# Kernel optimization log

Hardware: AMD Instinct MI355X
Metric: run time of the kernel (lower is better)

## Reference

```python
import jax, jax.numpy as jnp
import numpy as np

HIDDEN = 4096
NUM_HEADS = 32
NUM_KV_HEADS = 8
HEAD_DIM = 128
EPS = 1e-6
ROPE_THETA = 1000000.0
T = 2048


def setup_inputs() -> dict:
    key = jax.random.key(0)
    k1, k2, k3, k4, k5 = jax.random.split(key, 5)
    q_size = NUM_HEADS * HEAD_DIM
    kv_size = NUM_KV_HEADS * HEAD_DIM
    return {
        "positions": jnp.arange(T, dtype=jnp.int32),
        "hidden_states": jax.random.normal(k1, (T, HIDDEN), dtype=jnp.float32),
        "w_qkv": jax.random.normal(k2, (HIDDEN, q_size + 2 * kv_size), dtype=jnp.float32) * 0.02,
        "w_o": jax.random.normal(k3, (q_size, HIDDEN), dtype=jnp.float32) * 0.02,
        "q_norm_w": jnp.ones((HEAD_DIM,), dtype=jnp.float32) + 0.01 * jax.random.normal(k4, (HEAD_DIM,), dtype=jnp.float32),
        "k_norm_w": jnp.ones((HEAD_DIM,), dtype=jnp.float32) + 0.01 * jax.random.normal(k5, (HEAD_DIM,), dtype=jnp.float32),
    }


def _rms_norm(x, w, eps=EPS):
    # x: [..., head_dim], normalize over last dim
    var = jnp.mean(jnp.square(x), axis=-1, keepdims=True)
    return x * jax.lax.rsqrt(var + eps) * w


def _apply_rope(x, positions):
    # neox-style rotate-half RoPE, rotary_dim == head_dim
    d = x.shape[-1]
    inv_freq = 1.0 / (ROPE_THETA ** (jnp.arange(0, d, 2, dtype=jnp.float32) / d))
    freqs = positions.astype(jnp.float32)[:, None] * inv_freq[None, :]  # [T, d/2]
    cos = jnp.cos(freqs)[:, None, :]  # [T, 1, d/2]
    sin = jnp.sin(freqs)[:, None, :]
    x1, x2 = jnp.split(x, 2, axis=-1)
    return jnp.concatenate([x1 * cos - x2 * sin, x2 * cos + x1 * sin], axis=-1)


def reference(positions, hidden_states, w_qkv, w_o, q_norm_w, k_norm_w):
    num_tokens = hidden_states.shape[0]
    q_size = NUM_HEADS * HEAD_DIM
    kv_size = NUM_KV_HEADS * HEAD_DIM
    group = NUM_HEADS // NUM_KV_HEADS

    qkv = hidden_states @ w_qkv  # [T, q+2kv]
    q = qkv[:, :q_size].reshape(num_tokens, NUM_HEADS, HEAD_DIM)
    k = qkv[:, q_size:q_size + kv_size].reshape(num_tokens, NUM_KV_HEADS, HEAD_DIM)
    v = qkv[:, q_size + kv_size:].reshape(num_tokens, NUM_KV_HEADS, HEAD_DIM)

    q = _rms_norm(q, q_norm_w)
    k = _rms_norm(k, k_norm_w)
    q = _apply_rope(q, positions)
    k = _apply_rope(k, positions)

    scale = HEAD_DIM ** -0.5
    # GQA: group query heads over shared kv heads
    qg = q.reshape(num_tokens, NUM_KV_HEADS, group, HEAD_DIM)
    scores = jnp.einsum("tkgd,skd->kgts", qg * scale, k)  # [KH, G, T, S]
    causal = positions[:, None] >= positions[None, :]  # [T, S]
    scores = jnp.where(causal[None, None, :, :], scores, jnp.finfo(scores.dtype).min)
    probs = jax.nn.softmax(scores, axis=-1)
    out = jnp.einsum("kgts,skd->tkgd", probs, v)  # [T, KH, G, D]
    out = out.reshape(num_tokens, q_size)
    return out @ w_o
```

## Files before the change

kernel.cpp:

```cpp
#include <hip/hip_runtime.h>
#include <cstdint>
#include <cstddef>

#define T_TOK 2048
#define HID   4096
#define NQH   32
#define NKVH  8
#define HD    128
#define QKV_N 6144

typedef __bf16 bf16x8 __attribute__((ext_vector_type(8)));
typedef __bf16 bf16x4 __attribute__((ext_vector_type(4)));
typedef float  f32x4  __attribute__((ext_vector_type(4)));
typedef float  f32x16 __attribute__((ext_vector_type(16)));

#define AS1 __attribute__((address_space(1)))
#define AS3 __attribute__((address_space(3)))

__device__ __forceinline__ void gll16(const void* g, void* l) {
  __builtin_amdgcn_global_load_lds((const AS1 void*)g, (AS3 void*)l, 16, 0, 0);
}

__global__ __launch_bounds__(256) void k_convert(const float* __restrict__ in,
                                                 __bf16* __restrict__ out, int n4) {
  int i = blockIdx.x * 256 + threadIdx.x;
  if (i >= n4) return;
  float4 v = ((const float4*)in)[i];
  bf16x4 o;
  o[0] = (__bf16)v.x; o[1] = (__bf16)v.y; o[2] = (__bf16)v.z; o[3] = (__bf16)v.w;
  ((bf16x4*)out)[i] = o;
}

__global__ __launch_bounds__(256) void k_transpose(const float* __restrict__ in,
                                                   __bf16* __restrict__ out,
                                                   int R, int C) {
  __shared__ float tile[32][33];
  int c0 = blockIdx.x * 32, r0 = blockIdx.y * 32;
  int tx = threadIdx.x, ty = threadIdx.y;
#pragma unroll
  for (int k = 0; k < 4; ++k)
    tile[ty + k*8][tx] = in[(size_t)(r0 + ty + k*8) * C + c0 + tx];
  __syncthreads();
#pragma unroll
  for (int k = 0; k < 4; ++k)
    out[(size_t)(c0 + ty + k*8) * R + r0 + tx] = (__bf16)tile[tx][ty + k*8];
}

template <int NFR>
__global__ __launch_bounds__(512, 2) void k_gemm8(const __bf16* __restrict__ A,
                                                  const __bf16* __restrict__ Bt,
                                                  float* __restrict__ C,
                                                  int N, int K) {
  constexpr int BN   = 64 * NFR;
  constexpr int WN   = 16 * NFR;
  constexpr int NB   = NFR / 2;
  constexpr int NH   = NFR / 2;
  constexpr int BREG = BN * 64;
  constexpr int BUFSZ = 16384 + 2 * BREG;
  __shared__ alignas(16) char ldsb[2 * BUFSZ];
  const int tid = threadIdx.x;
  const int lane = tid & 63, w = tid >> 6;
  const int l16 = lane & 15, lg = lane >> 4;
  const int wm = w >> 2, wn = w & 3;

  const int x = blockIdx.x & 7, idx = blockIdx.x >> 3;
  const int bm = (x & 1) * 8 + (idx & 7);
  const int bn = (x >> 1) * 4 + (idx >> 3);

  const int rA = tid >> 2, pA = tid & 3;
  const __bf16* asrc = A + (size_t)(bm * 128 + rA) * K + ((pA ^ ((rA >> 1) & 3)) * 8);
  const __bf16* bsrc = Bt + (size_t)(bn * BN + rA) * K + ((pA ^ ((rA >> 1) & 3)) * 8);

#define RA_(buf, mk) (ldsb + (buf) * BUFSZ + (mk) * 8192)
#define RB_(buf, mk) (ldsb + (buf) * BUFSZ + 16384 + (mk) * BREG)
#define STG_A(buf, mk, kk) { gll16(asrc + (kk) + (mk) * 32, RA_(buf, mk) + w * 1024); }
#define STG_B(buf, mk, kk) { _Pragma("unroll") \
    for (int j = 0; j < NB; ++j) \
      gll16(bsrc + (size_t)j * 128 * K + (kk) + (mk) * 32, RB_(buf, mk) + j * 8192 + w * 1024); }
#define FRAG(base, row) (*(const bf16x8*)((base) + (row) * 64 + ((lg ^ (((row) >> 1) & 3)) << 4)))
#define WAITN() { if constexpr (NFR == 6) asm volatile("s_waitcnt vmcnt(4)" ::: "memory"); \
                  else                    asm volatile("s_waitcnt vmcnt(3)" ::: "memory"); }

  f32x4 acc[4][NFR] = {};
  const int nkt = K >> 6;

  STG_A(0, 0, 0); STG_B(0, 0, 0); STG_A(0, 1, 0); STG_B(0, 1, 0);

  for (int t = 0; t < nkt - 1; ++t) {
    const int cur = t & 1, nxt = cur ^ 1;
    const int kn = (t + 1) * 64;
    bf16x8 af[4], bf_[NH];

    STG_A(nxt, 0, kn);
    WAITN();
    __builtin_amdgcn_s_barrier();
    __builtin_amdgcn_sched_barrier(0);
#pragma unroll
    for (int i = 0; i < 4; ++i) af[i] = FRAG(RA_(cur, 0), wm * 64 + i * 16 + l16);
#pragma unroll
    for (int n = 0; n < NH; ++n) bf_[n] = FRAG(RB_(cur, 0), wn * WN + n * 16 + l16);
    __builtin_amdgcn_s_setprio(1);
#pragma unroll
    for (int i = 0; i < 4; ++i)
#pragma unroll
      for (int n = 0; n < NH; ++n)
        acc[i][n] = __builtin_amdgcn_mfma_f32_16x16x32_bf16(af[i], bf_[n], acc[i][n], 0, 0, 0);
    __builtin_amdgcn_s_setprio(0);
    __builtin_amdgcn_s_barrier();

#pragma unroll
    for (int n = 0; n < NH; ++n) bf_[n] = FRAG(RB_(cur, 0), wn * WN + (NH + n) * 16 + l16);
    STG_B(nxt, 0, kn);
    __builtin_amdgcn_s_barrier();
    __builtin_amdgcn_s_setprio(1);
#pragma unroll
    for (int i = 0; i < 4; ++i)
#pragma unroll
      for (int n = 0; n < NH; ++n)
        acc[i][NH + n] = __builtin_amdgcn_mfma_f32_16x16x32_bf16(af[i], bf_[n], acc[i][NH + n], 0, 0, 0);
    __builtin_amdgcn_s_setprio(0);
    __builtin_amdgcn_s_barrier();

    STG_A(nxt, 1, kn);
    WAITN();
    __builtin_amdgcn_s_barrier();
    __builtin_amdgcn_sched_barrier(0);
#pragma unroll
    for (int i = 0; i < 4; ++i) af[i] = FRAG(RA_(cur, 1), wm * 64 + i * 16 + l16);
#pragma unroll
    for (int n = 0; n < NH; ++n) bf_[n] = FRAG(RB_(cur, 1), wn * WN + n * 16 + l16);
    __builtin_amdgcn_s_setprio(1);
#pragma unroll
    for (int i = 0; i < 4; ++i)
#pragma unroll
      for (int n = 0; n < NH; ++n)
        acc[i][n] = __builtin_amdgcn_mfma_f32_16x16x32_bf16(af[i], bf_[n], acc[i][n], 0, 0, 0);
    __builtin_amdgcn_s_setprio(0);
    __builtin_amdgcn_s_barrier();

#pragma unroll
    for (int n = 0; n < NH; ++n) bf_[n] = FRAG(RB_(cur, 1), wn * WN + (NH + n) * 16 + l16);
    STG_B(nxt, 1, kn);
    __builtin_amdgcn_s_barrier();
    __builtin_amdgcn_s_setprio(1);
#pragma unroll
    for (int i = 0; i < 4; ++i)
#pragma unroll
      for (int n = 0; n < NH; ++n)
        acc[i][NH + n] = __builtin_amdgcn_mfma_f32_16x16x32_bf16(af[i], bf_[n], acc[i][NH + n], 0, 0, 0);
    __builtin_amdgcn_s_setprio(0);
    __builtin_amdgcn_s_barrier();
  }

  asm volatile("s_waitcnt vmcnt(0)" ::: "memory");
  __builtin_amdgcn_s_barrier();
  __builtin_amdgcn_sched_barrier(0);
  {
    const int cur = (nkt - 1) & 1;
#pragma unroll
    for (int mk = 0; mk < 2; ++mk) {
      bf16x8 aa[4], bb[NFR];
#pragma unroll
      for (int i = 0; i < 4; ++i) aa[i] = FRAG(RA_(cur, mk), wm * 64 + i * 16 + l16);
#pragma unroll
      for (int n = 0; n < NFR; ++n) bb[n] = FRAG(RB_(cur, mk), wn * WN + n * 16 + l16);
#pragma unroll
      for (int i = 0; i < 4; ++i)
#pragma unroll
        for (int n = 0; n < NFR; ++n)
          acc[i][n] = __builtin_amdgcn_mfma_f32_16x16x32_bf16(aa[i], bb[n], acc[i][n], 0, 0, 0);
    }
  }
#undef RA_
#undef RB_
#undef STG_A
#undef STG_B
#undef FRAG
#undef WAITN

#pragma unroll
  for (int mi = 0; mi < 4; ++mi)
#pragma unroll
    for (int ni = 0; ni < NFR; ++ni) {
      int row = bm * 128 + wm * 64 + mi * 16 + lg * 4;
      int col = bn * BN + wn * WN + ni * 16 + l16;
#pragma unroll
      for (int r = 0; r < 4; ++r)
        C[(size_t)(row + r) * N + col] = acc[mi][ni][r];
    }
}

__global__ __launch_bounds__(64) void k_norm_rope(const float* __restrict__ qkv,
                                                  const int* __restrict__ pos,
                                                  const float* __restrict__ qw,
                                                  const float* __restrict__ kw,
                                                  __bf16* __restrict__ qo,
                                                  __bf16* __restrict__ ko,
                                                  __bf16* __restrict__ vto) {
  const int slot = blockIdx.x;
  const int t    = blockIdx.y;
  const int i    = threadIdx.x;
  const int off  = (slot < 32) ? slot * 128
                 : (slot < 40) ? 4096 + (slot - 32) * 128
                                : 5120 + (slot - 40) * 128;
  const float* base = qkv + (size_t)t * QKV_N + off;
  float x1 = base[i], x2 = base[i + 64];
  if (slot >= 40) {
    __bf16* o = vto + ((size_t)(slot - 40) * HD) * T_TOK + t;
    o[(size_t)i * T_TOK] = (__bf16)x1;
    o[(size_t)(i + 64) * T_TOK] = (__bf16)x2;
    return;
  }
  float ss = x1 * x1 + x2 * x2;
#pragma unroll
  for (int m = 32; m >= 1; m >>= 1) ss += __shfl_xor(ss, m);
  float rinv = rsqrtf(ss * (1.0f / 128.0f) + 1e-6f);
  const float* wn = (slot < 32) ? qw : kw;
  float n1 = x1 * rinv * wn[i];
  float n2 = x2 * rinv * wn[i + 64];
  float fr = (float)pos[t] * expf((float)i * -0.21586735246819178f);
  float cs = cosf(fr), sn = sinf(fr);
  float o1 = n1 * cs - n2 * sn;
  float o2 = n2 * cs + n1 * sn;
  if (slot < 32) {
    const float QSC = 0.08838834764831845f * 1.4426950408889634f;
    __bf16* o = qo + ((size_t)t * NQH + slot) * HD;
    o[i] = (__bf16)(o1 * QSC);
    o[i + 64] = (__bf16)(o2 * QSC);
  } else {
    __bf16* o = ko + ((size_t)t * NKVH + (slot - 32)) * HD;
    o[i] = (__bf16)o1;
    o[i + 64] = (__bf16)o2;
  }
}

__global__ __launch_bounds__(256, 2) void k_attn(const __bf16* __restrict__ Q,
                                                 const __bf16* __restrict__ K,
                                                 const __bf16* __restrict__ Vt,
                                                 __bf16* __restrict__ O) {
  __shared__ alignas(16) __bf16 Ks[64 * 128];
  __shared__ alignas(16) __bf16 Vts[128 * 64];
  const int bid = blockIdx.x;
  const int kvh = bid & 7;
  const int qc  = bid >> 3;
  const int tid = threadIdx.x, lane = tid & 63, w = tid >> 6;
  const int l31 = lane & 31, hi = lane >> 5;
  const int h  = kvh * 4 + w;
  const int q0 = qc * 32;
  const int qrow = q0 + l31;
  char* Ksb = (char*)Ks;
  char* Vtb = (char*)Vts;

  bf16x8 qf[8];
  {
    const __bf16* qp = Q + ((size_t)qrow * NQH + h) * HD + hi * 8;
#pragma unroll
    for (int dc = 0; dc < 8; ++dc)
      qf[dc] = *(const bf16x8*)(qp + dc * 16);
  }

  size_t ksrc[4], vsrc[4];
#pragma unroll
  for (int j = 0; j < 4; ++j) {
    int kr = w * 16 + j * 4 + (lane >> 4);
    ksrc[j] = ((size_t)kr * NKVH + kvh) * HD + (size_t)(((lane & 15) ^ (kr & 15)) * 8);
    int vr = w * 32 + j * 8 + (lane >> 3);
    vsrc[j] = ((size_t)(kvh * HD + vr)) * T_TOK + (size_t)(((lane & 7) ^ (vr & 7)) * 8);
  }

  float m_run = -3.0e38f, l_run = 0.f;
  f32x16 ot[4] = {};

  const int ntiles = (qc >> 1) + 1;
  for (int tt = 0; tt < ntiles; ++tt) {
    const int s0 = tt * 64;
#pragma unroll
    for (int j = 0; j < 4; ++j) {
      gll16(K + (size_t)s0 * (NKVH * HD) + ksrc[j], Ksb + (w * 4 + j) * 1024);
      gll16(Vt + (size_t)s0 + vsrc[j], Vtb + (w * 4 + j) * 1024);
    }
    __syncthreads();

    f32x16 sac[2] = {};
#pragma unroll
    for (int hf = 0; hf < 2; ++hf) {
      int krow = hf * 32 + l31;
#pragma unroll
      for (int dc = 0; dc < 8; ++dc) {
        bf16x8 kf = *(const bf16x8*)(Ksb + krow * 256 + (((dc * 2 + hi) ^ (krow & 15)) * 16));
        sac[hf] = __builtin_amdgcn_mfma_f32_32x32x16_bf16(kf, qf[dc], sac[hf], 0, 0, 0);
      }
    }

    float pv[32];
    if (s0 + 64 > q0) {
#pragma unroll
      for (int hf = 0; hf < 2; ++hf)
#pragma unroll
        for (int r = 0; r < 16; ++r) {
          int kvg = s0 + hf * 32 + (r & 3) + ((r >> 2) * 8) + hi * 4;
          pv[hf * 16 + r] = (kvg > qrow) ? -3.0e38f : sac[hf][r];
        }
    } else {
#pragma unroll
      for (int hf = 0; hf < 2; ++hf)
#pragma unroll
        for (int r = 0; r < 16; ++r) pv[hf * 16 + r] = sac[hf][r];
    }
    float t16[16];
#pragma unroll
    for (int i = 0; i < 16; ++i) t16[i] = fmaxf(pv[i], pv[i + 16]);
#pragma unroll
    for (int i = 0; i < 8; ++i) t16[i] = fmaxf(t16[i], t16[i + 8]);
#pragma unroll
    for (int i = 0; i < 4; ++i) t16[i] = fmaxf(t16[i], t16[i + 4]);
    float mt = fmaxf(fmaxf(t16[0], t16[1]), fmaxf(t16[2], t16[3]));
    mt = fmaxf(mt, __shfl_xor(mt, 32));
    if (!__all(mt - m_run <= 10.0f)) {
      float m_new = fmaxf(m_run, mt);
      float corr = exp2f(m_run - m_new);
      l_run *= corr;
#pragma unroll
      for (int dt = 0; dt < 4; ++dt)
#pragma unroll
        for (int r = 0; r < 16; ++r) ot[dt][r] *= corr;
      m_run = m_new;
    }
#pragma unroll
    for (int i = 0; i < 32; ++i) pv[i] = exp2f(pv[i] - m_run);
#pragma unroll
    for (int i = 0; i < 16; ++i) t16[i] = pv[i] + pv[i + 16];
#pragma unroll
    for (int i = 0; i < 8; ++i) t16[i] += t16[i + 8];
#pragma unroll
    for (int i = 0; i < 4; ++i) t16[i] += t16[i + 4];
    float rs = (t16[0] + t16[1]) + (t16[2] + t16[3]);
    rs += __shfl_xor(rs, 32);
    l_run += rs;

    uint32_t wds[16];
#pragma unroll
    for (int i = 0; i < 16; ++i) {
      uint32_t r;
      asm("v_cvt_pk_bf16_f32 %0, %1, %2" : "=v"(r) : "v"(pv[2 * i]), "v"(pv[2 * i + 1]));
      wds[i] = r;
    }
#pragma unroll
    for (int c = 0; c < 4; ++c) {
      const int base = (c >> 1) * 8 + (c & 1) * 4;
      uint32_t sa = hi ? wds[base + 0] : wds[base + 2];
      uint32_t sb = hi ? wds[base + 1] : wds[base + 3];
      uint32_t ra = __shfl_xor(sa, 32);
      uint32_t rb = __shfl_xor(sb, 32);
      union { uint32_t u[4]; bf16x8 v; } pf;
      pf.u[0] = hi ? ra : wds[base + 0];
      pf.u[1] = hi ? rb : wds[base + 1];
      pf.u[2] = hi ? wds[base + 2] : ra;
      pf.u[3] = hi ? wds[base + 3] : rb;
#pragma unroll
      for (int dt = 0; dt < 4; ++dt) {
        int vrow = dt * 32 + l31;
        bf16x8 vf = *(const bf16x8*)(Vtb + vrow * 128 + (((c * 2 + hi) ^ (vrow & 7)) * 16));
        ot[dt] = __builtin_amdgcn_mfma_f32_32x32x16_bf16(vf, pf.v, ot[dt], 0, 0, 0);
      }
    }
    __syncthreads();
  }

  float inv = 1.0f / l_run;
  char* Ob = Ksb + w * 8192;
#pragma unroll
  for (int dt = 0; dt < 4; ++dt)
#pragma unroll
    for (int r = 0; r < 16; ++r) {
      int d = dt * 32 + (r & 3) + ((r >> 2) * 8) + hi * 4;
      *(__bf16*)(Ob + l31 * 256 + ((d * 2) ^ ((l31 & 7) << 4))) = (__bf16)(ot[dt][r] * inv);
    }
#pragma unroll
  for (int pass = 0; pass < 8; ++pass) {
    int q = pass * 4 + (lane >> 4);
    int ch = lane & 15;
    bf16x8 vvv = *(const bf16x8*)(Ob + q * 256 + ((ch ^ (q & 7)) * 16));
    *(bf16x8*)(O + ((size_t)(q0 + q) * NQH + h) * HD + ch * 8) = vvv;
  }
}

extern "C" void kernel_launch(void* const* d_in, const int* in_sizes, int n_in,
                              void* d_out, int out_size, void* d_ws, size_t ws_size,
                              hipStream_t stream) {
  const int*   positions = (const int*)d_in[0];
  const float* hidden    = (const float*)d_in[1];
  const float* w_qkv     = (const float*)d_in[2];
  const float* w_o       = (const float*)d_in[3];
  const float* q_norm    = (const float*)d_in[4];
  const float* k_norm    = (const float*)d_in[5];
  float* out = (float*)d_out;

  char* ws = (char*)d_ws;
  __bf16* wqkv_t   = (__bf16*)ws;
  __bf16* wo_t     = (__bf16*)(ws + 50331648);
  __bf16* hidden_b = (__bf16*)(ws + 83886080);
  float*  qkv      = (float*)(ws + 100663296);
  __bf16* qb  = (__bf16*)ws;
  __bf16* kb  = (__bf16*)(ws + 16777216);
  __bf16* vtb = (__bf16*)(ws + 20971520);
  __bf16* attn_o = hidden_b;

  k_convert<<<dim3((T_TOK * HID / 4 + 255) / 256), 256, 0, stream>>>(hidden, hidden_b, T_TOK * HID / 4);
  k_transpose<<<dim3(QKV_N / 32, HID / 32), dim3(32, 8), 0, stream>>>(w_qkv, wqkv_t, HID, QKV_N);
  k_transpose<<<dim3(HID / 32, HID / 32), dim3(32, 8), 0, stream>>>(w_o, wo_t, HID, HID);
  k_gemm8<6><<<dim3(256), 512, 0, stream>>>(hidden_b, wqkv_t, qkv, QKV_N, HID);
  k_norm_rope<<<dim3(48, T_TOK), 64, 0, stream>>>(qkv, positions, q_norm, k_norm, qb, kb, vtb);
  k_attn<<<dim3(512), 256, 0, stream>>>(qb, kb, vtb, attn_o);
  k_gemm8<4><<<dim3(256), 512, 0, stream>>>(attn_o, wo_t, out, HID, HID);
}
```

Measured before the change: 327.9 us.

## Vectorize weight transposes, split V transpose out, batch norm-rope per token

```diff
diff --git a/kernel.cpp b/kernel.cpp
--- a/kernel.cpp
+++ b/kernel.cpp
@@ -34,16 +34,48 @@
 __global__ __launch_bounds__(256) void k_transpose(const float* __restrict__ in,
                                                    __bf16* __restrict__ out,
                                                    int R, int C) {
-  __shared__ float tile[32][33];
-  int c0 = blockIdx.x * 32, r0 = blockIdx.y * 32;
-  int tx = threadIdx.x, ty = threadIdx.y;
-#pragma unroll
-  for (int k = 0; k < 4; ++k)
-    tile[ty + k*8][tx] = in[(size_t)(r0 + ty + k*8) * C + c0 + tx];
+  __shared__ float tile[64][33];
+  const int tid = threadIdx.x;
+  const int c0 = blockIdx.x * 32, r0 = blockIdx.y * 64;
+  const int ty = tid >> 3, tx = tid & 7;
+#pragma unroll
+  for (int k = 0; k < 2; ++k) {
+    float4 v = *(const float4*)&in[(size_t)(r0 + ty + k * 32) * C + c0 + tx * 4];
+    tile[ty + k * 32][tx * 4 + 0] = v.x;
+    tile[ty + k * 32][tx * 4 + 1] = v.y;
+    tile[ty + k * 32][tx * 4 + 2] = v.z;
+    tile[ty + k * 32][tx * 4 + 3] = v.w;
+  }
   __syncthreads();
-#pragma unroll
-  for (int k = 0; k < 4; ++k)
-    out[(size_t)(c0 + ty + k*8) * R + r0 + tx] = (__bf16)tile[tx][ty + k*8];
+  const int c = tid >> 3, rq = tid & 7;
+  bf16x8 o;
+#pragma unroll
+  for (int i = 0; i < 8; ++i) o[i] = (__bf16)tile[rq * 8 + i][c];
+  *(bf16x8*)&out[(size_t)(c0 + c) * R + r0 + rq * 8] = o;
+}
+
+__global__ __launch_bounds__(256) void k_vtrans(const float* __restrict__ qkv,
+                                                __bf16* __restrict__ vt) {
+  __shared__ float tile[64][33];
+  const int tid = threadIdx.x;
+  const int kvh = blockIdx.z;
+  const int d0 = blockIdx.x * 32;
+  const int t0 = blockIdx.y * 64;
+  const int ty = tid >> 3, tx = tid & 7;
+#pragma unroll
+  for (int k = 0; k < 2; ++k) {
+    float4 v = *(const float4*)&qkv[(size_t)(t0 + ty + k * 32) * QKV_N + 5120 + kvh * 128 + d0 + tx * 4];
+    tile[ty + k * 32][tx * 4 + 0] = v.x;
+    tile[ty + k * 32][tx * 4 + 1] = v.y;
+    tile[ty + k * 32][tx * 4 + 2] = v.z;
+    tile[ty + k * 32][tx * 4 + 3] = v.w;
+  }
+  __syncthreads();
+  const int d = tid >> 3, tq = tid & 7;
+  bf16x8 o;
+#pragma unroll
+  for (int i = 0; i < 8; ++i) o[i] = (__bf16)tile[tq * 8 + i][d];
+  *(bf16x8*)&vt[((size_t)kvh * 128 + d0 + d) * T_TOK + t0 + tq * 8] = o;
 }
 
 template <int NFR>
@@ -190,47 +222,43 @@
     }
 }
 
-__global__ __launch_bounds__(64) void k_norm_rope(const float* __restrict__ qkv,
-                                                  const int* __restrict__ pos,
-                                                  const float* __restrict__ qw,
-                                                  const float* __restrict__ kw,
-                                                  __bf16* __restrict__ qo,
-                                                  __bf16* __restrict__ ko,
-                                                  __bf16* __restrict__ vto) {
-  const int slot = blockIdx.x;
-  const int t    = blockIdx.y;
-  const int i    = threadIdx.x;
-  const int off  = (slot < 32) ? slot * 128
-                 : (slot < 40) ? 4096 + (slot - 32) * 128
-                                : 5120 + (slot - 40) * 128;
-  const float* base = qkv + (size_t)t * QKV_N + off;
-  float x1 = base[i], x2 = base[i + 64];
-  if (slot >= 40) {
-    __bf16* o = vto + ((size_t)(slot - 40) * HD) * T_TOK + t;
-    o[(size_t)i * T_TOK] = (__bf16)x1;
-    o[(size_t)(i + 64) * T_TOK] = (__bf16)x2;
-    return;
-  }
-  float ss = x1 * x1 + x2 * x2;
-#pragma unroll
-  for (int m = 32; m >= 1; m >>= 1) ss += __shfl_xor(ss, m);
-  float rinv = rsqrtf(ss * (1.0f / 128.0f) + 1e-6f);
-  const float* wn = (slot < 32) ? qw : kw;
-  float n1 = x1 * rinv * wn[i];
-  float n2 = x2 * rinv * wn[i + 64];
-  float fr = (float)pos[t] * expf((float)i * -0.21586735246819178f);
-  float cs = cosf(fr), sn = sinf(fr);
-  float o1 = n1 * cs - n2 * sn;
-  float o2 = n2 * cs + n1 * sn;
-  if (slot < 32) {
-    const float QSC = 0.08838834764831845f * 1.4426950408889634f;
-    __bf16* o = qo + ((size_t)t * NQH + slot) * HD;
-    o[i] = (__bf16)(o1 * QSC);
-    o[i + 64] = (__bf16)(o2 * QSC);
-  } else {
-    __bf16* o = ko + ((size_t)t * NKVH + (slot - 32)) * HD;
-    o[i] = (__bf16)o1;
-    o[i + 64] = (__bf16)o2;
+__global__ __launch_bounds__(256) void k_norm_rope(const float* __restrict__ qkv,
+                                                   const int* __restrict__ pos,
+                                                   const float* __restrict__ qw,
+                                                   const float* __restrict__ kw,
+                                                   __bf16* __restrict__ qo,
+                                                   __bf16* __restrict__ ko) {
+  const int t = blockIdx.x;
+  const int w = threadIdx.x >> 6, i = threadIdx.x & 63;
+  const float fr = (float)pos[t] * expf((float)i * -0.21586735246819178f);
+  const float cs = cosf(fr), sn = sinf(fr);
+  const float qwi1 = qw[i], qwi2 = qw[i + 64];
+  const float kwi1 = kw[i], kwi2 = kw[i + 64];
+  const float* base = qkv + (size_t)t * QKV_N;
+#pragma unroll
+  for (int s = 0; s < 10; ++s) {
+    const int slot = w * 10 + s;
+    const int off = (slot < 32) ? slot * 128 : 4096 + (slot - 32) * 128;
+    float x1 = base[off + i], x2 = base[off + i + 64];
+    float ss = x1 * x1 + x2 * x2;
+#pragma unroll
+    for (int m = 32; m >= 1; m >>= 1) ss += __shfl_xor(ss, m);
+    float rinv = rsqrtf(ss * (1.0f / 128.0f) + 1e-6f);
+    float n1, n2;
+    if (slot < 32) { n1 = x1 * rinv * qwi1; n2 = x2 * rinv * qwi2; }
+    else           { n1 = x1 * rinv * kwi1; n2 = x2 * rinv * kwi2; }
+    float o1 = n1 * cs - n2 * sn;
+    float o2 = n2 * cs + n1 * sn;
+    if (slot < 32) {
+      const float QSC = 0.08838834764831845f * 1.4426950408889634f;
+      __bf16* o = qo + ((size_t)t * NQH + slot) * HD;
+      o[i] = (__bf16)(o1 * QSC);
+      o[i + 64] = (__bf16)(o2 * QSC);
+    } else {
+      __bf16* o = ko + ((size_t)t * NKVH + (slot - 32)) * HD;
+      o[i] = (__bf16)o1;
+      o[i + 64] = (__bf16)o2;
+    }
   }
 }
 
@@ -407,10 +435,11 @@
   __bf16* attn_o = hidden_b;
 
   k_convert<<<dim3((T_TOK * HID / 4 + 255) / 256), 256, 0, stream>>>(hidden, hidden_b, T_TOK * HID / 4);
-  k_transpose<<<dim3(QKV_N / 32, HID / 32), dim3(32, 8), 0, stream>>>(w_qkv, wqkv_t, HID, QKV_N);
-  k_transpose<<<dim3(HID / 32, HID / 32), dim3(32, 8), 0, stream>>>(w_o, wo_t, HID, HID);
+  k_transpose<<<dim3(QKV_N / 32, HID / 64), 256, 0, stream>>>(w_qkv, wqkv_t, HID, QKV_N);
+  k_transpose<<<dim3(HID / 32, HID / 64), 256, 0, stream>>>(w_o, wo_t, HID, HID);
   k_gemm8<6><<<dim3(256), 512, 0, stream>>>(hidden_b, wqkv_t, qkv, QKV_N, HID);
-  k_norm_rope<<<dim3(48, T_TOK), 64, 0, stream>>>(qkv, positions, q_norm, k_norm, qb, kb, vtb);
+  k_norm_rope<<<dim3(T_TOK), 256, 0, stream>>>(qkv, positions, q_norm, k_norm, qb, kb);
+  k_vtrans<<<dim3(4, T_TOK / 64, NKVH), 256, 0, stream>>>(qkv, vtb);
   k_attn<<<dim3(512), 256, 0, stream>>>(qb, kb, vtb, attn_o);
   k_gemm8<4><<<dim3(256), 512, 0, stream>>>(attn_o, wo_t, out, HID, HID);
 }
```

New measurement: 319.0 us. -2.7%, faster.
